# Optimization experiments

Hardware: AMD Instinct MI355X
Metric: run time of the kernel (lower is better)

The kernel has to match this reference:

```python
import jax, jax.numpy as jnp
import numpy as np
import math

B, T, C = 1, 2048, 2048
N_HEAD = 32
N_QUERY_GROUPS = 8
HEAD_SIZE = 64
ROPE_N_ELEM = 16  # int(0.25 * 64)
Q_PER_KV = N_HEAD // N_QUERY_GROUPS  # 4
QKV_DIM = (N_HEAD + 2 * N_QUERY_GROUPS) * HEAD_SIZE  # 3072


def setup_inputs() -> dict:
    key = jax.random.key(0)
    ks = jax.random.split(key, 7)
    x = jax.random.normal(ks[0], (B, T, C), dtype=jnp.float32)
    # realistic rope tables
    inv_freq = 1.0 / (10000.0 ** (jnp.arange(0, ROPE_N_ELEM, 2, dtype=jnp.float32) / ROPE_N_ELEM))
    t = jnp.arange(T, dtype=jnp.float32)
    freqs = jnp.outer(t, inv_freq)                       # [T, rope/2]
    emb = jnp.concatenate([freqs, freqs], axis=-1)       # [T, rope]
    cos, sin = jnp.cos(emb), jnp.sin(emb)
    s = 0.02
    W_attn = jax.random.normal(ks[1], (QKV_DIM, C), dtype=jnp.float32) * s
    b_attn = jax.random.normal(ks[2], (QKV_DIM,), dtype=jnp.float32) * s
    W_proj = jax.random.normal(ks[3], (C, N_HEAD * HEAD_SIZE), dtype=jnp.float32) * s
    b_proj = jax.random.normal(ks[4], (C,), dtype=jnp.float32) * s
    return {"x": x, "cos": cos, "sin": sin, "W_attn": W_attn, "b_attn": b_attn,
            "W_proj": W_proj, "b_proj": b_proj}


def _apply_rope(t, cos, sin):
    # t: [B, H, T, rope]; cos/sin: [T, rope]
    half = t.shape[-1] // 2
    t1, t2 = t[..., :half], t[..., half:]
    rotated = jnp.concatenate([-t2, t1], axis=-1)
    return t * cos + rotated * sin


def reference(x, cos, sin, W_attn, b_attn, W_proj, b_proj):
    Bc, Tc, Cc = x.shape
    qkv = x @ W_attn.T + b_attn                                   # [B, T, 3072]
    qkv = qkv.reshape(Bc, Tc, N_QUERY_GROUPS, Q_PER_KV + 2, HEAD_SIZE)
    qkv = qkv.transpose(0, 2, 3, 1, 4)                            # [B, G, q_per_kv+2, T, hs]
    q = qkv[:, :, :Q_PER_KV]                                      # [B, G, q_per_kv, T, hs]
    k = qkv[:, :, Q_PER_KV:Q_PER_KV + 1]                          # [B, G, 1, T, hs]
    v = qkv[:, :, Q_PER_KV + 1:]
    # GQA expand (n_query_groups != n_head, prefill path)
    k = jnp.broadcast_to(k, (Bc, N_QUERY_GROUPS, Q_PER_KV, Tc, HEAD_SIZE))
    v = jnp.broadcast_to(v, (Bc, N_QUERY_GROUPS, Q_PER_KV, Tc, HEAD_SIZE))
    q = q.reshape(Bc, N_HEAD, Tc, HEAD_SIZE)
    k = k.reshape(Bc, N_HEAD, Tc, HEAD_SIZE)
    v = v.reshape(Bc, N_HEAD, Tc, HEAD_SIZE)
    # partial RoPE on first ROPE_N_ELEM dims
    q = jnp.concatenate([_apply_rope(q[..., :ROPE_N_ELEM], cos, sin), q[..., ROPE_N_ELEM:]], axis=-1)
    k = jnp.concatenate([_apply_rope(k[..., :ROPE_N_ELEM], cos, sin), k[..., ROPE_N_ELEM:]], axis=-1)
    # causal SDPA with scale 1/sqrt(head_size)
    scale = 1.0 / math.sqrt(HEAD_SIZE)
    scores = jnp.einsum('bhqd,bhkd->bhqk', q, k) * scale          # [B, H, T, T]
    causal = jnp.tril(jnp.ones((Tc, Tc), dtype=bool))
    scores = jnp.where(causal, scores, jnp.finfo(scores.dtype).min)
    attn = jax.nn.softmax(scores, axis=-1)
    y = jnp.einsum('bhqk,bhkd->bhqd', attn, v)                    # [B, H, T, hs]
    y = y.transpose(0, 2, 1, 3).reshape(Bc, Tc, N_HEAD * HEAD_SIZE)
    return y @ W_proj.T + b_proj
```

## Files before the change

### kernel.cpp

```cpp
#include <hip/hip_runtime.h>
#include <hip/hip_bf16.h>

using u16 = unsigned short;
typedef float f32x4 __attribute__((ext_vector_type(4)));
typedef __bf16 bf16x8 __attribute__((ext_vector_type(8)));

#define T_SEQ 2048
#define C_DIM 2048
#define QKV_DIM 3072
#define N_HEAD 32
#define N_GROUPS 8
#define HEAD_SIZE 64
#define ROPE_N 16
#define NEG_BIG (-1e30f)
#define LS 72

__device__ inline float bf2f(u16 u) {
    union { float f; unsigned v; } x; x.v = ((unsigned)u) << 16; return x.f;
}
__device__ inline u16 f2bf(float f) {
    __bf16 h = (__bf16)f;
    return *(u16*)&h;
}

__device__ __forceinline__ void gl_lds16(const u16* g, u16* l) {
    __builtin_amdgcn_global_load_lds(
        (const __attribute__((address_space(1))) unsigned int*)g,
        (__attribute__((address_space(3))) unsigned int*)l,
        16, 0, 0);
}

__global__ void detect_dtype(const u16* __restrict__ x, int* __restrict__ flag)
{
    __shared__ int s[256];
    int cnt = 0;
    for (int i = threadIdx.x; i < 8192; i += 256) {
        int e = (x[i] >> 7) & 0xFF;
        cnt += (e >= 0xC0);
    }
    s[threadIdx.x] = cnt;
    __syncthreads();
    if (threadIdx.x == 0) {
        int tot = 0;
        for (int i = 0; i < 256; i++) tot += s[i];
        flag[0] = (tot > 64) ? 1 : 0;
    }
}

struct ConvDesc {
    const void* src[7];
    u16*        dst[7];
    int         off8[8];
};

__global__ void convert_all(ConvDesc cd, const int* __restrict__ flag)
{
    int gid = blockIdx.x * blockDim.x + threadIdx.x;
    if (gid >= cd.off8[7]) return;
    int seg = 0;
#pragma unroll
    for (int s = 1; s < 7; s++) seg += (gid >= cd.off8[s]);
    int i = (gid - cd.off8[seg]) * 8;
    if (*flag) {
        const float4* s = (const float4*)((const float*)cd.src[seg] + i);
        float4 a = s[0], b = s[1];
        __attribute__((aligned(16))) u16 o[8] = {
            f2bf(a.x), f2bf(a.y), f2bf(a.z), f2bf(a.w),
            f2bf(b.x), f2bf(b.y), f2bf(b.z), f2bf(b.w) };
        *(int4*)(cd.dst[seg] + i) = *(const int4*)o;
    } else {
        *(int4*)(cd.dst[seg] + i) = *(const int4*)((const u16*)cd.src[seg] + i);
    }
}

__global__ __launch_bounds__(256) void gemm_qkv_rope(
    const u16* __restrict__ A, const u16* __restrict__ W,
    const u16* __restrict__ bias,
    const u16* __restrict__ ccos, const u16* __restrict__ csin,
    u16* __restrict__ Qout, u16* __restrict__ Kout, u16* __restrict__ Vtout)
{
    __shared__ __attribute__((aligned(16))) u16 lds_a[64 * 32];
    __shared__ __attribute__((aligned(16))) u16 lds_b[128 * 32];

    const int tid  = threadIdx.x;
    const int wave = tid >> 6;
    const int lane = tid & 63;
    const int quad = lane >> 4;
    const int l16  = lane & 15;
    const int bm = blockIdx.y * 64;
    const int bn = blockIdx.x * 128;
    const int K = C_DIM;

    f32x4 acc[4][2] = {};

    const int ra = tid >> 2,          ca = (tid & 3) * 8;
    const int rb0 = tid >> 2,         cb0 = (tid & 3) * 8;
    const int rb1 = (tid + 256) >> 2, cb1 = (tid & 3) * 8;

    for (int k0 = 0; k0 < K; k0 += 32) {
        __syncthreads();
        gl_lds16(A + (size_t)(bm + ra) * K + k0 + ca,  lds_a + tid * 8);
        gl_lds16(W + (size_t)(bn + rb0) * K + k0 + cb0, lds_b + tid * 8);
        gl_lds16(W + (size_t)(bn + rb1) * K + k0 + cb1, lds_b + (tid + 256) * 8);
        __syncthreads();

        bf16x8 afr[4], bfr[2];
#pragma unroll
        for (int i = 0; i < 4; i++)
            afr[i] = *(const bf16x8*)(lds_a + (i * 16 + l16) * 32 + quad * 8);
#pragma unroll
        for (int j = 0; j < 2; j++)
            bfr[j] = *(const bf16x8*)(lds_b + (wave * 32 + j * 16 + l16) * 32 + quad * 8);
#pragma unroll
        for (int i = 0; i < 4; i++)
#pragma unroll
            for (int j = 0; j < 2; j++)
                acc[i][j] = __builtin_amdgcn_mfma_f32_16x16x32_bf16(afr[i], bfr[j], acc[i][j], 0, 0, 0);
    }

#pragma unroll
    for (int j = 0; j < 2; j++) {
        const int colb = bn + wave * 32 + j * 16;
        const int col  = colb + l16;
        const int slot = (colb % 384) >> 6;
        const int g    = colb / 384;
        const int dbase = colb & 63;
        const int d    = dbase + l16;
        const float bv = bf2f(bias[col]);
        const bool rope = (dbase == 0) && (slot != 5);
#pragma unroll
        for (int i = 0; i < 4; i++) {
            const int trow = bm + i * 16 + quad * 4;
#pragma unroll
            for (int r = 0; r < 4; r++) {
                float v = acc[i][j][r] + bv;
                float outv = v;
                if (rope) {
                    float part = __shfl_xor(v, 8, 64);
                    float rot = (l16 < 8) ? -part : part;
                    float cc = bf2f(ccos[(trow + r) * ROPE_N + l16]);
                    float ss = bf2f(csin[(trow + r) * ROPE_N + l16]);
                    outv = v * cc + rot * ss;
                }
                const int t = trow + r;
                if (slot < 4) {
                    int hh = g * 4 + slot;
                    Qout[((size_t)hh * T_SEQ + t) * 64 + d] = f2bf(outv * 0.125f);
                } else if (slot == 4) {
                    Kout[((size_t)g * T_SEQ + t) * 64 + d] = f2bf(outv);
                } else {
                    Vtout[((size_t)g * 64 + d) * T_SEQ + t] = f2bf(outv);
                }
            }
        }
    }
}

__global__ __launch_bounds__(256) void gemm_bt(
    const u16* __restrict__ A, const u16* __restrict__ W,
    const u16* __restrict__ bias, u16* __restrict__ Cout,
    int M, int N, int K, const int* __restrict__ out_f32_flag)
{
    __shared__ __attribute__((aligned(16))) u16 lds_a[64 * 32];
    __shared__ __attribute__((aligned(16))) u16 lds_b[128 * 32];

    const int tid  = threadIdx.x;
    const int wave = tid >> 6;
    const int lane = tid & 63;
    const int quad = lane >> 4;
    const int l16  = lane & 15;
    const int bm = blockIdx.y * 64;
    const int bn = blockIdx.x * 128;

    f32x4 acc[4][2] = {};

    const int ra = tid >> 2,          ca = (tid & 3) * 8;
    const int rb1 = (tid + 256) >> 2;

    for (int k0 = 0; k0 < K; k0 += 32) {
        __syncthreads();
        gl_lds16(A + (size_t)(bm + ra) * K + k0 + ca,  lds_a + tid * 8);
        gl_lds16(W + (size_t)(bn + ra) * K + k0 + ca,  lds_b + tid * 8);
        gl_lds16(W + (size_t)(bn + rb1) * K + k0 + ca, lds_b + (tid + 256) * 8);
        __syncthreads();

        bf16x8 afr[4], bfr[2];
#pragma unroll
        for (int i = 0; i < 4; i++)
            afr[i] = *(const bf16x8*)(lds_a + (i * 16 + l16) * 32 + quad * 8);
#pragma unroll
        for (int j = 0; j < 2; j++)
            bfr[j] = *(const bf16x8*)(lds_b + (wave * 32 + j * 16 + l16) * 32 + quad * 8);
#pragma unroll
        for (int i = 0; i < 4; i++)
#pragma unroll
            for (int j = 0; j < 2; j++)
                acc[i][j] = __builtin_amdgcn_mfma_f32_16x16x32_bf16(afr[i], bfr[j], acc[i][j], 0, 0, 0);
    }

    const int of32 = out_f32_flag ? *out_f32_flag : 0;
#pragma unroll
    for (int i = 0; i < 4; i++) {
        int row = bm + i * 16 + quad * 4;
#pragma unroll
        for (int j = 0; j < 2; j++) {
            int col = bn + wave * 32 + j * 16 + l16;
            float bv = bf2f(bias[col]);
#pragma unroll
            for (int r = 0; r < 4; r++) {
                float v = acc[i][j][r] + bv;
                size_t idx = (size_t)(row + r) * N + col;
                if (of32) ((float*)Cout)[idx] = v;
                else      Cout[idx] = f2bf(v);
            }
        }
    }
}

__global__ __launch_bounds__(256) void flash_attn(
    const u16* __restrict__ Q, const u16* __restrict__ K,
    const u16* __restrict__ Vt, u16* __restrict__ Y)
{
    __shared__ __attribute__((aligned(16))) u16 lds_q[64 * LS];
    __shared__ __attribute__((aligned(16))) u16 lds_k[2][64 * LS];
    __shared__ __attribute__((aligned(16))) u16 lds_vt[2][64 * LS];
    __shared__ __attribute__((aligned(16))) u16 lds_p[4][16 * LS];

    const int h  = blockIdx.y;
    const int g  = h >> 2;
    const int tid  = threadIdx.x;
    const int wave = tid >> 6;
    const int lane = tid & 63;
    const int quad = lane >> 4;
    const int l16  = lane & 15;
    const int NQT = T_SEQ / 64;

    const u16* Qh = Q  + (size_t)h * T_SEQ * 64;
    const u16* Kg = K  + (size_t)g * T_SEQ * 64;
    const u16* Vg = Vt + (size_t)g * 64 * T_SEQ;

    const int srow = tid >> 3, scc = (tid & 7) * 8;

    int4 kr0, kr1, vr0, vr1;
    auto load_tile = [&](int k0) {
        kr0 = *(const int4*)(Kg + (size_t)(k0 + srow) * 64 + scc);
        kr1 = *(const int4*)(Kg + (size_t)(k0 + srow + 32) * 64 + scc);
        vr0 = *(const int4*)(Vg + (size_t)srow * T_SEQ + k0 + scc);
        vr1 = *(const int4*)(Vg + (size_t)(srow + 32) * T_SEQ + k0 + scc);
    };

    for (int pass = 0; pass < 2; pass++) {
        const int qt = pass ? (NQT - 1 - blockIdx.x) : blockIdx.x;
        const int q0 = qt * 64;

        __syncthreads();
        for (int s = tid; s < 512; s += 256) {
            int row = s >> 3, cc = (s & 7) * 8;
            *(int4*)(lds_q + row * LS + cc) =
                *(const int4*)(Qh + (size_t)(q0 + row) * 64 + cc);
        }
        __syncthreads();

        bf16x8 a_q[2];
#pragma unroll
        for (int ks = 0; ks < 2; ks++)
            a_q[ks] = *(const bf16x8*)(lds_q + (wave * 16 + l16) * LS + ks * 32 + quad * 8);

        float rs[4] = {0.f, 0.f, 0.f, 0.f};
        f32x4 o_acc[4] = {};

        load_tile(0);

        for (int kt = 0; kt <= qt; kt++) {
            const int p = kt & 1;
            *(int4*)(lds_k[p]  + srow * LS + scc)        = kr0;
            *(int4*)(lds_k[p]  + (srow + 32) * LS + scc) = kr1;
            *(int4*)(lds_vt[p] + srow * LS + scc)        = vr0;
            *(int4*)(lds_vt[p] + (srow + 32) * LS + scc) = vr1;
            __syncthreads();
            if (kt < qt) load_tile((kt + 1) * 64);

            f32x4 sc[4] = {};
#pragma unroll
            for (int ks = 0; ks < 2; ks++)
#pragma unroll
                for (int t = 0; t < 4; t++) {
                    bf16x8 bk = *(const bf16x8*)(lds_k[p] + (t * 16 + l16) * LS + ks * 32 + quad * 8);
                    sc[t] = __builtin_amdgcn_mfma_f32_16x16x32_bf16(a_q[ks], bk, sc[t], 0, 0, 0);
                }

            if (kt == qt) {
                const int row_g = q0 + wave * 16 + quad * 4;
                const int k0 = kt * 64;
#pragma unroll
                for (int t = 0; t < 4; t++) {
                    int col_g = k0 + t * 16 + l16;
#pragma unroll
                    for (int r = 0; r < 4; r++)
                        if (col_g > row_g + r) sc[t][r] = NEG_BIG;
                }
            }

#pragma unroll
            for (int t = 0; t < 4; t++) {
                int colo = t * 16 + l16;
#pragma unroll
                for (int r = 0; r < 4; r++) {
                    float pv = __expf(sc[t][r]);
                    rs[r] += pv;
                    lds_p[wave][(quad * 4 + r) * LS + colo] = f2bf(pv);
                }
            }
            __syncthreads();

#pragma unroll
            for (int ks = 0; ks < 2; ks++) {
                bf16x8 ap = *(const bf16x8*)(lds_p[wave] + l16 * LS + ks * 32 + quad * 8);
#pragma unroll
                for (int t = 0; t < 4; t++) {
                    bf16x8 bv = *(const bf16x8*)(lds_vt[p] + (t * 16 + l16) * LS + ks * 32 + quad * 8);
                    o_acc[t] = __builtin_amdgcn_mfma_f32_16x16x32_bf16(ap, bv, o_acc[t], 0, 0, 0);
                }
            }
        }

#pragma unroll
        for (int off = 1; off < 16; off <<= 1)
#pragma unroll
            for (int r = 0; r < 4; r++)
                rs[r] += __shfl_xor(rs[r], off, 64);

#pragma unroll
        for (int t = 0; t < 4; t++)
#pragma unroll
            for (int r = 0; r < 4; r++) {
                int row = q0 + wave * 16 + quad * 4 + r;
                int d   = t * 16 + l16;
                Y[(size_t)row * (N_HEAD * HEAD_SIZE) + h * 64 + d] = f2bf(o_acc[t][r] / rs[r]);
            }
    }
}

extern "C" void kernel_launch(void* const* d_in, const int* in_sizes, int n_in,
                              void* d_out, int out_size, void* d_ws, size_t ws_size,
                              hipStream_t stream)
{
    int* flag = (int*)d_ws;
    u16* base = (u16*)d_ws + 8;

    u16* cx   = base;
    u16* cWa  = cx  + (size_t)T_SEQ * C_DIM;
    u16* cba  = cWa + (size_t)QKV_DIM * C_DIM;
    u16* cWp  = cba + QKV_DIM;
    u16* cbp  = cWp + (size_t)C_DIM * C_DIM;
    u16* ccos = cbp + C_DIM;
    u16* csin = ccos + (size_t)T_SEQ * ROPE_N;
    u16* Qb   = csin + (size_t)T_SEQ * ROPE_N;
    u16* Kb   = Qb + (size_t)N_HEAD * T_SEQ * HEAD_SIZE;
    u16* Vtb  = Kb + (size_t)N_GROUPS * T_SEQ * HEAD_SIZE;
    u16* Yb   = Vtb + (size_t)N_GROUPS * T_SEQ * HEAD_SIZE;

    dim3 blk(256);

    detect_dtype<<<1, blk, 0, stream>>>((const u16*)d_in[0], flag);

    ConvDesc cd;
    const int sizes[7] = { T_SEQ * C_DIM, T_SEQ * ROPE_N, T_SEQ * ROPE_N,
                           QKV_DIM * C_DIM, QKV_DIM, C_DIM * C_DIM, C_DIM };
    u16* dsts[7] = { cx, ccos, csin, cWa, cba, cWp, cbp };
    int acc8 = 0;
    for (int i = 0; i < 7; i++) {
        cd.src[i] = d_in[i];
        cd.dst[i] = dsts[i];
        cd.off8[i] = acc8;
        acc8 += sizes[i] / 8;
    }
    cd.off8[7] = acc8;
    convert_all<<<dim3((acc8 + 255) / 256), blk, 0, stream>>>(cd, flag);

    gemm_qkv_rope<<<dim3(QKV_DIM / 128, T_SEQ / 64), blk, 0, stream>>>(
        cx, cWa, cba, ccos, csin, Qb, Kb, Vtb);
    flash_attn<<<dim3(T_SEQ / 128, N_HEAD), blk, 0, stream>>>(Qb, Kb, Vtb, Yb);
    gemm_bt<<<dim3(C_DIM / 128, T_SEQ / 64), blk, 0, stream>>>(
        Yb, cWp, cbp, (u16*)d_out, T_SEQ, C_DIM, N_HEAD * HEAD_SIZE, flag);
}
```

Measured before the change: 275.2 us.

## Enlarge QKV GEMM tile, inline dtype detection, drop attention P barrier

The QKV+RoPE GEMM now uses a 128x128 block tile with a 2x2 wave layout and 4x4 MFMA accumulators per wave. This improves operand reuse and halves the number of blocks. The separate dtype-detection kernel and its workspace flag are removed. Instead, every thread of the convert and output-projection kernels re-reads a 512-byte probe of x and recomputes the fp32 check, which adds redundant loads per thread. The block-wide __syncthreads between writing the per-wave P tile and the PV MFMA in flash attention is removed, relying on each wave only reading its own LDS slice.

```diff
diff --git a/kernel.cpp b/kernel.cpp
--- a/kernel.cpp
+++ b/kernel.cpp
@@ -22,6 +22,25 @@
     __bf16 h = (__bf16)f;
     return *(u16*)&h;
 }
+__device__ inline int4 cvt8(int4 lo, int4 hi) {
+    const float* fa = (const float*)&lo;
+    const float* fb = (const float*)&hi;
+    __attribute__((aligned(16))) u16 o[8] = {
+        f2bf(fa[0]), f2bf(fa[1]), f2bf(fa[2]), f2bf(fa[3]),
+        f2bf(fb[0]), f2bf(fb[1]), f2bf(fb[2]), f2bf(fb[3]) };
+    return *(const int4*)o;
+}
+
+__device__ __forceinline__ int detect_fp32(const unsigned* __restrict__ xw) {
+    int cnt = 0;
+#pragma unroll
+    for (int i = 0; i < 128; i++) {
+        unsigned w = xw[i];
+        cnt += (((w >> 7)  & 0xFF) >= 0xC0);
+        cnt += (((w >> 23) & 0xFF) >= 0xC0);
+    }
+    return cnt > 8;
+}
 
 __device__ __forceinline__ void gl_lds16(const u16* g, u16* l) {
     __builtin_amdgcn_global_load_lds(
@@ -30,44 +49,24 @@
         16, 0, 0);
 }
 
-__global__ void detect_dtype(const u16* __restrict__ x, int* __restrict__ flag)
-{
-    __shared__ int s[256];
-    int cnt = 0;
-    for (int i = threadIdx.x; i < 8192; i += 256) {
-        int e = (x[i] >> 7) & 0xFF;
-        cnt += (e >= 0xC0);
-    }
-    s[threadIdx.x] = cnt;
-    __syncthreads();
-    if (threadIdx.x == 0) {
-        int tot = 0;
-        for (int i = 0; i < 256; i++) tot += s[i];
-        flag[0] = (tot > 64) ? 1 : 0;
-    }
-}
-
 struct ConvDesc {
     const void* src[7];
     u16*        dst[7];
     int         off8[8];
 };
 
-__global__ void convert_all(ConvDesc cd, const int* __restrict__ flag)
-{
+__global__ void convert_all(ConvDesc cd)
+{
+    const int fl = detect_fp32((const unsigned*)cd.src[0]);
     int gid = blockIdx.x * blockDim.x + threadIdx.x;
     if (gid >= cd.off8[7]) return;
     int seg = 0;
 #pragma unroll
     for (int s = 1; s < 7; s++) seg += (gid >= cd.off8[s]);
     int i = (gid - cd.off8[seg]) * 8;
-    if (*flag) {
+    if (fl) {
         const float4* s = (const float4*)((const float*)cd.src[seg] + i);
-        float4 a = s[0], b = s[1];
-        __attribute__((aligned(16))) u16 o[8] = {
-            f2bf(a.x), f2bf(a.y), f2bf(a.z), f2bf(a.w),
-            f2bf(b.x), f2bf(b.y), f2bf(b.z), f2bf(b.w) };
-        *(int4*)(cd.dst[seg] + i) = *(const int4*)o;
+        *(int4*)(cd.dst[seg] + i) = cvt8(*(const int4*)&s[0], *(const int4*)&s[1]);
     } else {
         *(int4*)(cd.dst[seg] + i) = *(const int4*)((const u16*)cd.src[seg] + i);
     }
@@ -79,7 +78,7 @@
     const u16* __restrict__ ccos, const u16* __restrict__ csin,
     u16* __restrict__ Qout, u16* __restrict__ Kout, u16* __restrict__ Vtout)
 {
-    __shared__ __attribute__((aligned(16))) u16 lds_a[64 * 32];
+    __shared__ __attribute__((aligned(16))) u16 lds_a[128 * 32];
     __shared__ __attribute__((aligned(16))) u16 lds_b[128 * 32];
 
     const int tid  = threadIdx.x;
@@ -87,40 +86,42 @@
     const int lane = tid & 63;
     const int quad = lane >> 4;
     const int l16  = lane & 15;
-    const int bm = blockIdx.y * 64;
+    const int wr = wave >> 1, wc = wave & 1;
+    const int bm = blockIdx.y * 128;
     const int bn = blockIdx.x * 128;
     const int K = C_DIM;
 
-    f32x4 acc[4][2] = {};
-
-    const int ra = tid >> 2,          ca = (tid & 3) * 8;
-    const int rb0 = tid >> 2,         cb0 = (tid & 3) * 8;
-    const int rb1 = (tid + 256) >> 2, cb1 = (tid & 3) * 8;
+    f32x4 acc[4][4] = {};
+
+    const int s0 = tid, s1 = tid + 256;
+    const int r0 = s0 >> 2, c0 = (s0 & 3) * 8;
+    const int r1 = s1 >> 2, c1 = (s1 & 3) * 8;
 
     for (int k0 = 0; k0 < K; k0 += 32) {
         __syncthreads();
-        gl_lds16(A + (size_t)(bm + ra) * K + k0 + ca,  lds_a + tid * 8);
-        gl_lds16(W + (size_t)(bn + rb0) * K + k0 + cb0, lds_b + tid * 8);
-        gl_lds16(W + (size_t)(bn + rb1) * K + k0 + cb1, lds_b + (tid + 256) * 8);
-        __syncthreads();
-
-        bf16x8 afr[4], bfr[2];
+        gl_lds16(A + (size_t)(bm + r0) * K + k0 + c0, lds_a + s0 * 8);
+        gl_lds16(A + (size_t)(bm + r1) * K + k0 + c1, lds_a + s1 * 8);
+        gl_lds16(W + (size_t)(bn + r0) * K + k0 + c0, lds_b + s0 * 8);
+        gl_lds16(W + (size_t)(bn + r1) * K + k0 + c1, lds_b + s1 * 8);
+        __syncthreads();
+
+        bf16x8 afr[4], bfr[4];
 #pragma unroll
         for (int i = 0; i < 4; i++)
-            afr[i] = *(const bf16x8*)(lds_a + (i * 16 + l16) * 32 + quad * 8);
-#pragma unroll
-        for (int j = 0; j < 2; j++)
-            bfr[j] = *(const bf16x8*)(lds_b + (wave * 32 + j * 16 + l16) * 32 + quad * 8);
+            afr[i] = *(const bf16x8*)(lds_a + (wr * 64 + i * 16 + l16) * 32 + quad * 8);
+#pragma unroll
+        for (int j = 0; j < 4; j++)
+            bfr[j] = *(const bf16x8*)(lds_b + (wc * 64 + j * 16 + l16) * 32 + quad * 8);
 #pragma unroll
         for (int i = 0; i < 4; i++)
 #pragma unroll
-            for (int j = 0; j < 2; j++)
+            for (int j = 0; j < 4; j++)
                 acc[i][j] = __builtin_amdgcn_mfma_f32_16x16x32_bf16(afr[i], bfr[j], acc[i][j], 0, 0, 0);
     }
 
 #pragma unroll
-    for (int j = 0; j < 2; j++) {
-        const int colb = bn + wave * 32 + j * 16;
+    for (int j = 0; j < 4; j++) {
+        const int colb = bn + wc * 64 + j * 16;
         const int col  = colb + l16;
         const int slot = (colb % 384) >> 6;
         const int g    = colb / 384;
@@ -130,7 +131,7 @@
         const bool rope = (dbase == 0) && (slot != 5);
 #pragma unroll
         for (int i = 0; i < 4; i++) {
-            const int trow = bm + i * 16 + quad * 4;
+            const int trow = bm + wr * 64 + i * 16 + quad * 4;
 #pragma unroll
             for (int r = 0; r < 4; r++) {
                 float v = acc[i][j][r] + bv;
@@ -159,7 +160,7 @@
 __global__ __launch_bounds__(256) void gemm_bt(
     const u16* __restrict__ A, const u16* __restrict__ W,
     const u16* __restrict__ bias, u16* __restrict__ Cout,
-    int M, int N, int K, const int* __restrict__ out_f32_flag)
+    int M, int N, int K, const unsigned* __restrict__ xprobe)
 {
     __shared__ __attribute__((aligned(16))) u16 lds_a[64 * 32];
     __shared__ __attribute__((aligned(16))) u16 lds_b[128 * 32];
@@ -171,10 +172,11 @@
     const int l16  = lane & 15;
     const int bm = blockIdx.y * 64;
     const int bn = blockIdx.x * 128;
+    const int fl = detect_fp32(xprobe);
 
     f32x4 acc[4][2] = {};
 
-    const int ra = tid >> 2,          ca = (tid & 3) * 8;
+    const int ra = tid >> 2, ca = (tid & 3) * 8;
     const int rb1 = (tid + 256) >> 2;
 
     for (int k0 = 0; k0 < K; k0 += 32) {
@@ -198,7 +200,6 @@
                 acc[i][j] = __builtin_amdgcn_mfma_f32_16x16x32_bf16(afr[i], bfr[j], acc[i][j], 0, 0, 0);
     }
 
-    const int of32 = out_f32_flag ? *out_f32_flag : 0;
 #pragma unroll
     for (int i = 0; i < 4; i++) {
         int row = bm + i * 16 + quad * 4;
@@ -210,8 +211,8 @@
             for (int r = 0; r < 4; r++) {
                 float v = acc[i][j][r] + bv;
                 size_t idx = (size_t)(row + r) * N + col;
-                if (of32) ((float*)Cout)[idx] = v;
-                else      Cout[idx] = f2bf(v);
+                if (fl) ((float*)Cout)[idx] = v;
+                else    Cout[idx] = f2bf(v);
             }
         }
     }
@@ -311,15 +312,14 @@
                     lds_p[wave][(quad * 4 + r) * LS + colo] = f2bf(pv);
                 }
             }
-            __syncthreads();
 
 #pragma unroll
             for (int ks = 0; ks < 2; ks++) {
-                bf16x8 ap = *(const bf16x8*)(lds_p[wave] + l16 * LS + ks * 32 + quad * 8);
+                bf16x8 apf = *(const bf16x8*)(lds_p[wave] + l16 * LS + ks * 32 + quad * 8);
 #pragma unroll
                 for (int t = 0; t < 4; t++) {
-                    bf16x8 bv = *(const bf16x8*)(lds_vt[p] + (t * 16 + l16) * LS + ks * 32 + quad * 8);
-                    o_acc[t] = __builtin_amdgcn_mfma_f32_16x16x32_bf16(ap, bv, o_acc[t], 0, 0, 0);
+                    bf16x8 bvf = *(const bf16x8*)(lds_vt[p] + (t * 16 + l16) * LS + ks * 32 + quad * 8);
+                    o_acc[t] = __builtin_amdgcn_mfma_f32_16x16x32_bf16(apf, bvf, o_acc[t], 0, 0, 0);
                 }
             }
         }
@@ -345,8 +345,7 @@
                               void* d_out, int out_size, void* d_ws, size_t ws_size,
                               hipStream_t stream)
 {
-    int* flag = (int*)d_ws;
-    u16* base = (u16*)d_ws + 8;
+    u16* base = (u16*)d_ws;
 
     u16* cx   = base;
     u16* cWa  = cx  + (size_t)T_SEQ * C_DIM;
@@ -362,8 +361,6 @@
 
     dim3 blk(256);
 
-    detect_dtype<<<1, blk, 0, stream>>>((const u16*)d_in[0], flag);
-
     ConvDesc cd;
     const int sizes[7] = { T_SEQ * C_DIM, T_SEQ * ROPE_N, T_SEQ * ROPE_N,
                            QKV_DIM * C_DIM, QKV_DIM, C_DIM * C_DIM, C_DIM };
@@ -376,11 +373,12 @@
         acc8 += sizes[i] / 8;
     }
     cd.off8[7] = acc8;
-    convert_all<<<dim3((acc8 + 255) / 256), blk, 0, stream>>>(cd, flag);
-
-    gemm_qkv_rope<<<dim3(QKV_DIM / 128, T_SEQ / 64), blk, 0, stream>>>(
+    convert_all<<<dim3((acc8 + 255) / 256), blk, 0, stream>>>(cd);
+
+    gemm_qkv_rope<<<dim3(QKV_DIM / 128, T_SEQ / 128), blk, 0, stream>>>(
         cx, cWa, cba, ccos, csin, Qb, Kb, Vtb);
     flash_attn<<<dim3(T_SEQ / 128, N_HEAD), blk, 0, stream>>>(Qb, Kb, Vtb, Yb);
     gemm_bt<<<dim3(C_DIM / 128, T_SEQ / 64), blk, 0, stream>>>(
-        Yb, cWp, cbp, (u16*)d_out, T_SEQ, C_DIM, N_HEAD * HEAD_SIZE, flag);
-}
+        Yb, cWp, cbp, (u16*)d_out, T_SEQ, C_DIM, N_HEAD * HEAD_SIZE,
+        (const unsigned*)d_in[0]);
+}
```

Result: no change. 272.1 us (-1.2%).
